# Performance work log

Hardware: AMD Instinct MI355X
Metric: run time of the kernel (lower is better)

## Reference

```python
import jax, jax.numpy as jnp
import numpy as np

N, E = 50000, 200000
EMB_ATOM, EMB_EDGE = 256, 512
IN_SIZE = 2 * EMB_ATOM + EMB_EDGE  # 1024


def setup_inputs() -> dict:
    key = jax.random.key(0)
    k_h, k_m, k_i, k_j, k_w = jax.random.split(key, 5)
    h = jax.random.normal(k_h, (N, EMB_ATOM), dtype=jnp.float32)
    m_ij = jax.random.normal(k_m, (E, EMB_EDGE), dtype=jnp.float32)
    idx_i = jax.random.randint(k_i, (E,), 0, N, dtype=jnp.int64)
    idx_j = jax.random.randint(k_j, (E,), 0, N, dtype=jnp.int64)
    # bias-free Dense weight, stored as (in, out) for x @ W
    W = jax.random.normal(k_w, (IN_SIZE, EMB_EDGE), dtype=jnp.float32) * (1.0 / np.sqrt(IN_SIZE))
    return {"h": h, "m_ij": m_ij, "idx_i": idx_i, "idx_j": idx_j, "W": W}


def reference(h, m_ij, idx_i, idx_j, W):
    h_i = h[idx_i]                                   # (E, emb_atom)
    h_j = h[idx_j]                                   # (E, emb_atom)
    x = jnp.concatenate([h_i, h_j, m_ij], axis=-1)   # (E, 2*emb_atom + emb_edge)
    out = x @ W                                      # (E, emb_edge), bias-free Dense
    return jax.nn.silu(out)
```

## Files before the change

kernel.cpp:

```cpp
#include <hip/hip_runtime.h>
#include <hip/hip_bf16.h>
#include <math.h>

#define EMB_ATOM 256
#define EMB_EDGE 512
#define K_TOT    1024

typedef __attribute__((ext_vector_type(8))) short bf16x8;
typedef __attribute__((ext_vector_type(4))) float f32x4;
typedef struct { unsigned short x, y, z, w; } us4;

static __device__ __forceinline__ unsigned short f2bf(float f) {
  union { float f; unsigned u; } x; x.f = f;
  unsigned r = x.u + 0x7fffu + ((x.u >> 16) & 1u);
  return (unsigned short)(r >> 16);
}
static __device__ __forceinline__ float bf2f(unsigned short b) {
  union { unsigned u; float f; } x; x.u = ((unsigned)b) << 16; return x.f;
}
static __device__ __forceinline__ us4 f4bf(float4 v) {
  us4 o; o.x = f2bf(v.x); o.y = f2bf(v.y); o.z = f2bf(v.z); o.w = f2bf(v.w); return o;
}
static __device__ __forceinline__ bf16x8 cvt8(float4 a, float4 b) {
  union { bf16x8 v; __hip_bfloat162 h[4]; } u;
  u.h[0] = __float22bfloat162_rn(make_float2(a.x, a.y));
  u.h[1] = __float22bfloat162_rn(make_float2(a.z, a.w));
  u.h[2] = __float22bfloat162_rn(make_float2(b.x, b.y));
  u.h[3] = __float22bfloat162_rn(make_float2(b.z, b.w));
  return u.v;
}
static __device__ __forceinline__ void gload_lds16(const void* g, void* l) {
  __builtin_amdgcn_global_load_lds(
      (const __attribute__((address_space(1))) unsigned int*)g,
      (__attribute__((address_space(3))) unsigned int*)l, 16, 0, 0);
}
static __device__ __forceinline__ float silu_f(float x) { return x / (1.f + __expf(-x)); }

__global__ __launch_bounds__(256) void cvt_h_kernel(const float* __restrict__ h,
                                                    unsigned short* __restrict__ hb, int n4) {
  int i = blockIdx.x * 256 + threadIdx.x;
  if (i >= n4) return;
  const float4 v = ((const float4*)h)[i];
  ((us4*)hb)[i] = f4bf(v);
}

__global__ __launch_bounds__(256) void cvt_wh_kernel(const float* __restrict__ W,
                                                     unsigned short* __restrict__ Wt_h) {
  int o = blockIdx.x * 256 + threadIdx.x;
  int c = o >> 8, k = o & 255;
  float v = (c < 512) ? W[(size_t)k * EMB_EDGE + c]
                      : W[(size_t)(256 + k) * EMB_EDGE + (c - 512)];
  Wt_h[o] = f2bf(v);
}

__global__ __launch_bounds__(256) void cvt_wm_kernel(const float* __restrict__ W,
                                                     unsigned short* __restrict__ Wt_m) {
  int o = blockIdx.x * 256 + threadIdx.x;
  int c = o >> 9, k = o & 511;
  Wt_m[o] = f2bf(W[(size_t)(512 + k) * EMB_EDGE + c]);
}

__global__ __launch_bounds__(256) void hgemm_kernel(
    const unsigned short* __restrict__ hb,
    const unsigned short* __restrict__ Wt_h,
    unsigned short* __restrict__ H12, int N)
{
  __shared__ unsigned short As[2][128 * 64];
  __shared__ unsigned short Bs[2][128 * 64];
  const int bn = blockIdx.x;
  const int bm = blockIdx.y;
  const int row0 = bm * 128;
  const int tid = threadIdx.x, wave = tid >> 6, lane = tid & 63;
  const int srow = lane >> 3;
  const int schunk = ((lane & 7) ^ srow) * 8;

  size_t abase[4]; size_t bbase[4];
#pragma unroll
  for (int i = 0; i < 4; ++i) {
    int r = wave * 32 + i * 8 + srow;
    int e = row0 + r; if (e >= N) e = N - 1;
    abase[i] = (size_t)e * EMB_ATOM;
    bbase[i] = (size_t)(bn * 128 + r) * EMB_ATOM;
  }

  const int wr = wave >> 1, wc = wave & 1, fr = lane & 15, fq = lane >> 4;
  const int fs = fr & 7;

  f32x4 acc[4][4];
#pragma unroll
  for (int m = 0; m < 4; ++m)
#pragma unroll
    for (int n = 0; n < 4; ++n) acc[m][n] = (f32x4)0.f;

#pragma unroll
  for (int i = 0; i < 4; ++i) {
    gload_lds16(hb + abase[i] + schunk,   &As[0][(wave * 32 + i * 8) * 64 + lane * 8]);
    gload_lds16(Wt_h + bbase[i] + schunk, &Bs[0][(wave * 32 + i * 8) * 64 + lane * 8]);
  }
  __syncthreads();

  int cur = 0;
  for (int kt = 0; kt < 4; ++kt) {
    int nxt = cur ^ 1;
    if (kt < 3) {
      int kk = (kt + 1) * 64;
#pragma unroll
      for (int i = 0; i < 4; ++i) {
        gload_lds16(hb + abase[i] + kk + schunk,   &As[nxt][(wave * 32 + i * 8) * 64 + lane * 8]);
        gload_lds16(Wt_h + bbase[i] + kk + schunk, &Bs[nxt][(wave * 32 + i * 8) * 64 + lane * 8]);
      }
    }
#pragma unroll
    for (int ks = 0; ks < 2; ++ks) {
      bf16x8 a[4], b[4];
#pragma unroll
      for (int m = 0; m < 4; ++m)
        a[m] = *(const bf16x8*)(&As[cur][(wr * 64 + m * 16 + fr) * 64 + (((ks * 4 + fq) ^ fs) << 3)]);
#pragma unroll
      for (int n = 0; n < 4; ++n)
        b[n] = *(const bf16x8*)(&Bs[cur][(wc * 64 + n * 16 + fr) * 64 + (((ks * 4 + fq) ^ fs) << 3)]);
#pragma unroll
      for (int m = 0; m < 4; ++m)
#pragma unroll
        for (int n = 0; n < 4; ++n)
          acc[m][n] = __builtin_amdgcn_mfma_f32_16x16x32_bf16(a[m], b[n], acc[m][n], 0, 0, 0);
    }
    __syncthreads();
    cur = nxt;
  }

#pragma unroll
  for (int m = 0; m < 4; ++m) {
    int er0 = row0 + wr * 64 + m * 16 + fq * 4;
#pragma unroll
    for (int n = 0; n < 4; ++n) {
      int col = bn * 128 + wc * 64 + n * 16 + fr;
      f32x4 v = acc[m][n];
#pragma unroll
      for (int j = 0; j < 4; ++j) {
        int e = er0 + j;
        if (e < N) H12[(size_t)e * 1024 + col] = f2bf(v[j]);
      }
    }
  }
}

__global__ __launch_bounds__(256, 3) void mgemm_kernel(
    const float* __restrict__ m_ij,
    const int* __restrict__ idx_i,
    const int* __restrict__ idx_j,
    const unsigned short* __restrict__ Wt_m,
    const unsigned short* __restrict__ H12,
    float* __restrict__ out, int E, int nbm)
{
  __shared__ __align__(16) float          As[128 * 64];
  __shared__ __align__(16) unsigned short Bs[128 * 64];

  int b  = blockIdx.x;
  int bm = (b >> 5) * 8 + (b & 7);
  int bn = (b >> 3) & 3;
  if (bm >= nbm) return;
  const int row0 = bm * 128;
  const int tid = threadIdx.x, wave = tid >> 6, lane = tid & 63;
  const int fr = lane & 15, fq = lane >> 4;
  const int wr = wave >> 1, wc = wave & 1;

  const float* asrc[8];
#pragma unroll
  for (int i = 0; i < 8; ++i) {
    int r = wave * 32 + i * 4 + (lane >> 4);
    int e = row0 + r; if (e >= E) e = E - 1;
    int sc = (lane & 15) ^ (r & 15);
    asrc[i] = m_ij + (size_t)e * EMB_EDGE + sc * 4;
  }
  const unsigned short* bsrc[4];
#pragma unroll
  for (int i = 0; i < 4; ++i) {
    int r = wave * 32 + i * 8 + (lane >> 3);
    int sc = (lane & 7) ^ (r & 7);
    bsrc[i] = Wt_m + (size_t)(bn * 128 + r) * 512 + sc * 8;
  }

  f32x4 acc[4][4];
#pragma unroll
  for (int m = 0; m < 4; ++m)
#pragma unroll
    for (int n = 0; n < 4; ++n) acc[m][n] = (f32x4)0.f;

  for (int kt = 0; kt < 8; ++kt) {
    const int kk = kt * 64;
#pragma unroll
    for (int i = 0; i < 8; ++i)
      gload_lds16(asrc[i] + kk, &As[(wave * 32 + i * 4) * 64]);
#pragma unroll
    for (int i = 0; i < 4; ++i)
      gload_lds16(bsrc[i] + kk, &Bs[(wave * 32 + i * 8) * 64]);
    __syncthreads();

#pragma unroll
    for (int ks = 0; ks < 2; ++ks) {
      bf16x8 bfr[4];
#pragma unroll
      for (int n = 0; n < 4; ++n)
        bfr[n] = *(const bf16x8*)(&Bs[(wc * 64 + n * 16 + fr) * 64 + (((ks * 4 + fq) ^ (fr & 7)) << 3)]);
#pragma unroll
      for (int m = 0; m < 4; ++m) {
        const int row = wr * 64 + m * 16 + fr;
        const int L0  = ks * 8 + fq * 2;
        float4 c0 = *(const float4*)(&As[row * 64 + ((L0 ^ fr) << 2)]);
        float4 c1 = *(const float4*)(&As[row * 64 + (((L0 + 1) ^ fr) << 2)]);
        bf16x8 afr = cvt8(c0, c1);
#pragma unroll
        for (int n = 0; n < 4; ++n)
          acc[m][n] = __builtin_amdgcn_mfma_f32_16x16x32_bf16(afr, bfr[n], acc[m][n], 0, 0, 0);
      }
    }
    __syncthreads();
  }

#pragma unroll
  for (int m = 0; m < 4; ++m) {
#pragma unroll
    for (int j = 0; j < 4; ++j) {
      int e = row0 + wr * 64 + m * 16 + fq * 4 + j;
      if (e < E) {
        size_t gi = (size_t)idx_i[e] * 1024;
        size_t gj = (size_t)idx_j[e] * 1024 + 512;
#pragma unroll
        for (int n = 0; n < 4; ++n) {
          int col = bn * 128 + wc * 64 + n * 16 + fr;
          float x = acc[m][n][j] + bf2f(H12[gi + col]) + bf2f(H12[gj + col]);
          out[(size_t)e * EMB_EDGE + col] = silu_f(x);
        }
      }
    }
  }
}

__global__ __launch_bounds__(256) void cvt_wt_kernel(const float* __restrict__ W,
                                                     unsigned short* __restrict__ Wt) {
  int o = blockIdx.x * 256 + threadIdx.x;
  int n = o >> 10, k = o & 1023;
  Wt[o] = f2bf(W[(size_t)k * EMB_EDGE + n]);
}

__global__ __launch_bounds__(256) void gemm_gather_kernel(
    const unsigned short* __restrict__ hb,
    const float* __restrict__ m_ij,
    const int* __restrict__ idx_i,
    const int* __restrict__ idx_j,
    const unsigned short* __restrict__ Wt,
    float* __restrict__ out, int E)
{
  __shared__ unsigned short As[128 * 64];
  __shared__ unsigned short Bs[128 * 64];
  const int bn = blockIdx.x, bm = blockIdx.y;
  const int tid = threadIdx.x, wave = tid >> 6, lane = tid & 63;
  const int row0 = bm * 128;
  const int srow = lane >> 3, scol = (lane & 7) * 8;
  int arow[4], aii[4], ajj[4];
#pragma unroll
  for (int i = 0; i < 4; ++i) {
    int r = wave * 32 + i * 8 + srow;
    int e = row0 + r; if (e >= E) e = E - 1;
    arow[i] = r; aii[i] = idx_i[e]; ajj[i] = idx_j[e];
  }
  const int wr = wave >> 1, wc = wave & 1, fr = lane & 15, fq = lane >> 4;
  f32x4 acc[4][4];
#pragma unroll
  for (int m = 0; m < 4; ++m)
#pragma unroll
    for (int n = 0; n < 4; ++n) acc[m][n] = (f32x4)0.f;
  for (int kt = 0; kt < 16; ++kt) {
    __syncthreads();
#pragma unroll
    for (int i = 0; i < 4; ++i) {
      int nl = wave * 32 + i * 8 + srow;
      gload_lds16(Wt + (size_t)(bn * 128 + nl) * K_TOT + kt * 64 + scol, &Bs[nl * 64 + scol]);
    }
    if (kt < 8) {
      const int kh = (kt & 3) * 64;
#pragma unroll
      for (int i = 0; i < 4; ++i) {
        int idx = (kt < 4) ? aii[i] : ajj[i];
        gload_lds16(hb + (size_t)idx * EMB_ATOM + kh + scol, &As[arow[i] * 64 + scol]);
      }
    } else {
      const int kk = (kt - 8) * 64;
#pragma unroll
      for (int it = 0; it < 8; ++it) {
        int flat = it * 1024 + tid * 4;
        int r = flat >> 6, c = flat & 63;
        int e = row0 + r; if (e >= E) e = E - 1;
        const float4 v = *(const float4*)(m_ij + (size_t)e * EMB_EDGE + kk + c);
        *(us4*)(&As[r * 64 + c]) = f4bf(v);
      }
    }
    __syncthreads();
#pragma unroll
    for (int ks = 0; ks < 2; ++ks) {
      bf16x8 a[4], b[4];
#pragma unroll
      for (int m = 0; m < 4; ++m)
        a[m] = *(const bf16x8*)(&As[(wr * 64 + m * 16 + fr) * 64 + ks * 32 + fq * 8]);
#pragma unroll
      for (int n = 0; n < 4; ++n)
        b[n] = *(const bf16x8*)(&Bs[(wc * 64 + n * 16 + fr) * 64 + ks * 32 + fq * 8]);
#pragma unroll
      for (int m = 0; m < 4; ++m)
#pragma unroll
        for (int n = 0; n < 4; ++n)
          acc[m][n] = __builtin_amdgcn_mfma_f32_16x16x32_bf16(a[m], b[n], acc[m][n], 0, 0, 0);
    }
  }
#pragma unroll
  for (int m = 0; m < 4; ++m) {
    int er0 = row0 + wr * 64 + m * 16 + fq * 4;
#pragma unroll
    for (int n = 0; n < 4; ++n) {
      int col = bn * 128 + wc * 64 + n * 16 + fr;
      f32x4 v = acc[m][n];
#pragma unroll
      for (int j = 0; j < 4; ++j) {
        int e = er0 + j;
        if (e < E) out[(size_t)e * EMB_EDGE + col] = silu_f(v[j]);
      }
    }
  }
}

extern "C" void kernel_launch(void* const* d_in, const int* in_sizes, int n_in,
                              void* d_out, int out_size, void* d_ws, size_t ws_size,
                              hipStream_t stream) {
  const float* h    = (const float*)d_in[0];
  const float* m_ij = (const float*)d_in[1];
  const int*   ii   = (const int*)d_in[2];
  const int*   jj   = (const int*)d_in[3];
  const float* W    = (const float*)d_in[4];
  float* out = (float*)d_out;

  const int hsz = in_sizes[0];
  const int N   = hsz / EMB_ATOM;
  const int E   = in_sizes[2];

  unsigned short* hb   = (unsigned short*)d_ws;
  unsigned short* Wt_h = hb + hsz;
  unsigned short* Wt_m = Wt_h + 1024 * 256;
  unsigned short* H12  = Wt_m + 512 * 512;
  size_t need = ((size_t)hsz + 1024 * 256 + 512 * 512 + (size_t)N * 1024) * 2;

  if (ws_size >= need) {
    cvt_h_kernel<<<(hsz / 4 + 255) / 256, 256, 0, stream>>>(h, hb, hsz / 4);
    cvt_wh_kernel<<<1024, 256, 0, stream>>>(W, Wt_h);
    cvt_wm_kernel<<<1024, 256, 0, stream>>>(W, Wt_m);
    int nbmh = (N + 127) / 128;
    hgemm_kernel<<<dim3(8, nbmh), 256, 0, stream>>>(hb, Wt_h, H12, N);
    int nbm  = (E + 127) / 128;
    int ngrp = (nbm + 7) / 8;
    mgemm_kernel<<<ngrp * 32, 256, 0, stream>>>(m_ij, ii, jj, Wt_m, H12, out, E, nbm);
  } else {
    unsigned short* Wt  = (unsigned short*)d_ws;
    unsigned short* hbf = Wt + 512 * 1024;
    cvt_wt_kernel<<<(512 * 1024) / 256, 256, 0, stream>>>(W, Wt);
    cvt_h_kernel<<<(hsz / 4 + 255) / 256, 256, 0, stream>>>(h, hbf, hsz / 4);
    dim3 grid(4, (E + 127) / 128);
    gemm_gather_kernel<<<grid, 256, 0, stream>>>(hbf, m_ij, ii, jj, Wt, out, E);
  }
}
```

Measured before the change: 453.7 us.

## Prefetch m_ij into registers, store bf16 A tile, double-buffer W tile

The m_ij GEMM kernel now loads the next K-tile of m_ij into registers while the current tile is being computed, converts it to bf16 once, and writes it to LDS as bf16 instead of staging fp32 and converting per MFMA fragment. The W tile is double-buffered with async global-to-LDS loads issued one iteration ahead, and explicit barriers and waitcnts replace __syncthreads. The aim is to overlap global loads with MFMA work and to halve A-tile LDS footprint and traffic. In exchange the kernel uses more registers for the prefetch buffers and relies on hand-tuned waitcnt values that must match the number of outstanding loads.

```diff
diff --git a/kernel.cpp b/kernel.cpp
--- a/kernel.cpp
+++ b/kernel.cpp
@@ -153,8 +153,8 @@
     const unsigned short* __restrict__ H12,
     float* __restrict__ out, int E, int nbm)
 {
-  __shared__ __align__(16) float          As[128 * 64];
-  __shared__ __align__(16) unsigned short Bs[128 * 64];
+  __shared__ __align__(16) unsigned short As[128 * 64];
+  __shared__ __align__(16) unsigned short Bs[2][128 * 64];
 
   int b  = blockIdx.x;
   int bm = (b >> 5) * 8 + (b & 7);
@@ -165,20 +165,18 @@
   const int fr = lane & 15, fq = lane >> 4;
   const int wr = wave >> 1, wc = wave & 1;
 
-  const float* asrc[8];
-#pragma unroll
-  for (int i = 0; i < 8; ++i) {
-    int r = wave * 32 + i * 4 + (lane >> 4);
-    int e = row0 + r; if (e >= E) e = E - 1;
-    int sc = (lane & 15) ^ (r & 15);
-    asrc[i] = m_ij + (size_t)e * EMB_EDGE + sc * 4;
-  }
+  const int ar = tid >> 1;
+  const int ah = tid & 1;
+  int ae = row0 + ar; if (ae >= E) ae = E - 1;
+  const float* aptr = m_ij + (size_t)ae * EMB_EDGE + ah * 32;
   const unsigned short* bsrc[4];
+  unsigned bdst[4];
 #pragma unroll
   for (int i = 0; i < 4; ++i) {
     int r = wave * 32 + i * 8 + (lane >> 3);
     int sc = (lane & 7) ^ (r & 7);
     bsrc[i] = Wt_m + (size_t)(bn * 128 + r) * 512 + sc * 8;
+    bdst[i] = (wave * 32 + i * 8) * 64;
   }
 
   f32x4 acc[4][4];
@@ -187,35 +185,56 @@
 #pragma unroll
     for (int n = 0; n < 4; ++n) acc[m][n] = (f32x4)0.f;
 
+  float4 ra[8];
+#pragma unroll
+  for (int i = 0; i < 4; ++i) {
+    ra[2 * i]     = *(const float4*)(aptr + i * 8);
+    ra[2 * i + 1] = *(const float4*)(aptr + i * 8 + 4);
+  }
+#pragma unroll
+  for (int i = 0; i < 4; ++i) gload_lds16(bsrc[i], &Bs[0][bdst[i]]);
+
+#pragma unroll
   for (int kt = 0; kt < 8; ++kt) {
-    const int kk = kt * 64;
-#pragma unroll
-    for (int i = 0; i < 8; ++i)
-      gload_lds16(asrc[i] + kk, &As[(wave * 32 + i * 4) * 64]);
+    bf16x8 aw[4];
+#pragma unroll
+    for (int i = 0; i < 4; ++i) aw[i] = cvt8(ra[2 * i], ra[2 * i + 1]);
+    const int kkn = (kt < 7 ? kt + 1 : 7) * 64;
+#pragma unroll
+    for (int i = 0; i < 4; ++i) {
+      ra[2 * i]     = *(const float4*)(aptr + kkn + i * 8);
+      ra[2 * i + 1] = *(const float4*)(aptr + kkn + i * 8 + 4);
+    }
+    __builtin_amdgcn_sched_barrier(0);
+    __builtin_amdgcn_s_barrier();
+    __builtin_amdgcn_sched_barrier(0);
 #pragma unroll
     for (int i = 0; i < 4; ++i)
-      gload_lds16(bsrc[i] + kk, &Bs[(wave * 32 + i * 8) * 64]);
-    __syncthreads();
-
+      *(bf16x8*)(&As[ar * 64 + (((ah * 4 + i) ^ (ar & 7)) << 3)]) = aw[i];
+#pragma unroll
+    for (int i = 0; i < 4; ++i) gload_lds16(bsrc[i] + kkn, &Bs[(kt + 1) & 1][bdst[i]]);
+    __builtin_amdgcn_sched_barrier(0);
+    asm volatile("s_waitcnt lgkmcnt(0)" ::: "memory");
+    asm volatile("s_waitcnt vmcnt(12)" ::: "memory");
+    __builtin_amdgcn_sched_barrier(0);
+    __builtin_amdgcn_s_barrier();
+    __builtin_amdgcn_sched_barrier(0);
 #pragma unroll
     for (int ks = 0; ks < 2; ++ks) {
-      bf16x8 bfr[4];
+      bf16x8 afr[4], bfr[4];
 #pragma unroll
       for (int n = 0; n < 4; ++n)
-        bfr[n] = *(const bf16x8*)(&Bs[(wc * 64 + n * 16 + fr) * 64 + (((ks * 4 + fq) ^ (fr & 7)) << 3)]);
-#pragma unroll
-      for (int m = 0; m < 4; ++m) {
-        const int row = wr * 64 + m * 16 + fr;
-        const int L0  = ks * 8 + fq * 2;
-        float4 c0 = *(const float4*)(&As[row * 64 + ((L0 ^ fr) << 2)]);
-        float4 c1 = *(const float4*)(&As[row * 64 + (((L0 + 1) ^ fr) << 2)]);
-        bf16x8 afr = cvt8(c0, c1);
+        bfr[n] = *(const bf16x8*)(&Bs[kt & 1][(wc * 64 + n * 16 + fr) * 64 + (((ks * 4 + fq) ^ (fr & 7)) << 3)]);
+#pragma unroll
+      for (int m = 0; m < 4; ++m)
+        afr[m] = *(const bf16x8*)(&As[(wr * 64 + m * 16 + fr) * 64 + (((ks * 4 + fq) ^ (fr & 7)) << 3)]);
+#pragma unroll
+      for (int m = 0; m < 4; ++m)
 #pragma unroll
         for (int n = 0; n < 4; ++n)
-          acc[m][n] = __builtin_amdgcn_mfma_f32_16x16x32_bf16(afr, bfr[n], acc[m][n], 0, 0, 0);
-      }
-    }
-    __syncthreads();
+          acc[m][n] = __builtin_amdgcn_mfma_f32_16x16x32_bf16(afr[m], bfr[n], acc[m][n], 0, 0, 0);
+    }
+    __builtin_amdgcn_sched_barrier(0);
   }
 
 #pragma unroll
```

New measurement: 536.5 us. 1.18x slower.
